# Performance work log

Measured on AMD Instinct MI355X. Metric: run time of the kernel, lower is better.

## Reference

```python
import jax, jax.numpy as jnp
import numpy as np

B, T, TRAIN = 4, 2048, 1536
D, H, L, FF, V = 512, 8, 12, 2048, 100
DH = D // H
ROPE_BASE = 100000.0


def layer_norm(x, g, b, eps=1e-5):
    mu = jnp.mean(x, axis=-1, keepdims=True)
    var = jnp.mean(jnp.square(x - mu), axis=-1, keepdims=True)
    return (x - mu) * jax.lax.rsqrt(var + eps) * g + b


def rope_cos_sin(t, dh):
    inv_freq = 1.0 / (ROPE_BASE ** (jnp.arange(0, dh, 2, dtype=jnp.float32) / dh))  # (dh/2,)
    ang = jnp.arange(t, dtype=jnp.float32)[:, None] * inv_freq[None, :]  # (T, dh/2)
    return jnp.cos(ang), jnp.sin(ang)


def apply_rope_interleaved(x, cos, sin):
    # x: (B, T, H, DH); interleaved pairs (x0,x1),(x2,x3),...
    x1, x2 = x[..., 0::2], x[..., 1::2]
    c, s = cos[None, :, None, :], sin[None, :, None, :]
    r1 = x1 * c - x2 * s
    r2 = x1 * s + x2 * c
    return jnp.stack([r1, r2], axis=-1).reshape(x.shape)


def setup_inputs() -> dict:
    key = jax.random.key(0)
    ks = jax.random.split(key, 20)
    sc = 0.02
    inp = {
        'R': jax.random.normal(ks[0], (B, T, D), jnp.float32),
        'y_train': jax.random.randint(ks[1], (B, TRAIN), 0, V),
        'emb': jax.random.normal(ks[2], (V, D), jnp.float32) * sc,
        'Wqkv': jax.random.normal(ks[3], (L, D, 3 * D), jnp.float32) * sc,
        'bqkv': jnp.zeros((L, 3 * D), jnp.float32),
        'Wo': jax.random.normal(ks[4], (L, D, D), jnp.float32) * sc,
        'bo': jnp.zeros((L, D), jnp.float32),
        'ln1_g': jnp.ones((L, D), jnp.float32),
        'ln1_b': jnp.zeros((L, D), jnp.float32),
        'ln2_g': jnp.ones((L, D), jnp.float32),
        'ln2_b': jnp.zeros((L, D), jnp.float32),
        'W1': jax.random.normal(ks[5], (L, D, FF), jnp.float32) * sc,
        'b1': jnp.zeros((L, FF), jnp.float32),
        'W2': jax.random.normal(ks[6], (L, FF, D), jnp.float32) * sc,
        'b2': jnp.zeros((L, D), jnp.float32),
        'pW1': jax.random.normal(ks[7], (D, 2 * D), jnp.float32) * sc,
        'pb1': jnp.zeros((2 * D,), jnp.float32),
        'pW2': jax.random.normal(ks[8], (2 * D, V), jnp.float32) * sc,
        'pb2': jnp.zeros((V,), jnp.float32),
    }
    return inp


def icl_forward(R, y_train, emb, Wqkv, bqkv, Wo, bo, ln1_g, ln1_b, ln2_g, ln2_b, W1, b1, W2, b2, pW1, pb1, pW2, pb2):
    b, t, d = R.shape
    train = y_train.shape[1]
    # label embedding: train rows get emb[y], test rows get zeros
    y_emb = jnp.concatenate([emb[y_train], jnp.zeros((b, t - train, d), R.dtype)], axis=1)
    rep = R + y_emb
    # ICL mask: column j visible iff j < train or j == i
    idx = jnp.arange(t)
    allowed = (idx[None, :] < train) | (idx[:, None] == idx[None, :])
    mask = jnp.where(allowed, 0.0, -jnp.inf).astype(R.dtype)  # (T, T)
    cos, sin = rope_cos_sin(t, DH)
    scale = 1.0 / jnp.sqrt(jnp.asarray(DH, R.dtype))

    def block(x, p):
        wqkv, bq, wo, bob, g1, be1, g2, be2, w1, bb1, w2, bb2 = p
        h = layer_norm(x, g1, be1)
        qkv = h @ wqkv + bq  # (B,T,3D)
        q, k, v = jnp.split(qkv, 3, axis=-1)
        q = q.reshape(b, t, H, DH)
        k = k.reshape(b, t, H, DH)
        v = v.reshape(b, t, H, DH)
        q = apply_rope_interleaved(q, cos, sin)
        k = apply_rope_interleaved(k, cos, sin)
        scores = jnp.einsum('bthd,bshd->bhts', q, k) * scale + mask
        attn = jax.nn.softmax(scores, axis=-1)
        o = jnp.einsum('bhts,bshd->bthd', attn, v).reshape(b, t, d)
        x = x + o @ wo + bob
        h2 = layer_norm(x, g2, be2)
        x = x + jax.nn.gelu(h2 @ w1 + bb1) @ w2 + bb2
        return x, None

    rep, _ = jax.lax.scan(block, rep, (Wqkv, bqkv, Wo, bo, ln1_g, ln1_b, ln2_g, ln2_b, W1, b1, W2, b2))
    test = rep[:, train:, :]
    logits = jax.nn.gelu(test @ pW1 + pb1) @ pW2 + pb2  # (B, test, V)
    return logits


def reference(R, y_train, emb, Wqkv, bqkv, Wo, bo, ln1_g, ln1_b, ln2_g, ln2_b, W1, b1, W2, b2, pW1, pb1, pW2, pb2):
    return icl_forward(R, y_train, emb, Wqkv, bqkv, Wo, bo, ln1_g, ln1_b, ln2_g, ln2_b, W1, b1, W2, b2, pW1, pb1, pW2, pb2)
```

## Files before the change

### kernel.cpp

```cpp
#include <hip/hip_runtime.h>
#include <hip/hip_bf16.h>

#define BB 4
#define TT 2048
#define TRAIN 1536
#define DD 512
#define HH 8
#define LL 12
#define FFD 2048
#define VV 100
#define DH 64
#define NT (BB*TT)
#define NTEST (BB*(TT-TRAIN))

typedef __bf16 bf16x8 __attribute__((ext_vector_type(8)));
typedef float  f32x4  __attribute__((ext_vector_type(4)));

#define GLDS16(g, l) __builtin_amdgcn_global_load_lds( \
    (const __attribute__((address_space(1))) void*)(g), \
    (__attribute__((address_space(3))) void*)(l), 16, 0, 0)

__global__ __launch_bounds__(256) void emb_add(const float* __restrict__ R,
                                               const int* __restrict__ y,
                                               const float* __restrict__ emb,
                                               float* __restrict__ rep) {
    int idx = blockIdx.x * 256 + threadIdx.x;
    int d = idx & 511;
    int n = idx >> 9;
    int t = n & (TT - 1);
    int b = n >> 11;
    float val = R[idx];
    if (t < TRAIN) {
        int tok = y[b * TRAIN + t];
        val += emb[(size_t)tok * DD + d];
    }
    rep[idx] = val;
}

__global__ __launch_bounds__(256) void ln_wave(const float* __restrict__ x,
                                               const float* __restrict__ g,
                                               const float* __restrict__ bta,
                                               __bf16* __restrict__ out) {
    int row = blockIdx.x * 4 + (threadIdx.x >> 6);
    int lane = threadIdx.x & 63;
    const float* xr = x + (size_t)row * DD + lane * 8;
    float4 a = *(const float4*)xr;
    float4 c = *(const float4*)(xr + 4);
    float s  = a.x + a.y + a.z + a.w + c.x + c.y + c.z + c.w;
    float sq = a.x*a.x + a.y*a.y + a.z*a.z + a.w*a.w + c.x*c.x + c.y*c.y + c.z*c.z + c.w*c.w;
#pragma unroll
    for (int off = 1; off < 64; off <<= 1) {
        s  += __shfl_xor(s, off);
        sq += __shfl_xor(sq, off);
    }
    float mu  = s * (1.0f / DD);
    float var = sq * (1.0f / DD) - mu * mu;
    float inv = rsqrtf(var + 1e-5f);
    const float* gp = g + lane * 8;
    const float* bp = bta + lane * 8;
    float4 g0 = *(const float4*)gp, g1 = *(const float4*)(gp + 4);
    float4 b0 = *(const float4*)bp, b1 = *(const float4*)(bp + 4);
    __bf16 o8[8];
    o8[0] = (__bf16)((a.x - mu) * inv * g0.x + b0.x);
    o8[1] = (__bf16)((a.y - mu) * inv * g0.y + b0.y);
    o8[2] = (__bf16)((a.z - mu) * inv * g0.z + b0.z);
    o8[3] = (__bf16)((a.w - mu) * inv * g0.w + b0.w);
    o8[4] = (__bf16)((c.x - mu) * inv * g1.x + b1.x);
    o8[5] = (__bf16)((c.y - mu) * inv * g1.y + b1.y);
    o8[6] = (__bf16)((c.z - mu) * inv * g1.z + b1.z);
    o8[7] = (__bf16)((c.w - mu) * inv * g1.w + b1.w);
    *(uint4*)(out + (size_t)row * DD + lane * 8) = *(uint4*)o8;
}

__global__ __launch_bounds__(256) void rope_tab(float* __restrict__ ctab, float* __restrict__ stab) {
    int idx = blockIdx.x * 256 + threadIdx.x;
    int p = idx & 31, t = idx >> 5;
    double freq = exp(-((double)(2 * p) / 64.0) * log(100000.0));
    double ang = (double)t * freq;
    ctab[idx] = (float)cos(ang);
    stab[idx] = (float)sin(ang);
}

__global__ __launch_bounds__(256) void rope_vt(const __bf16* __restrict__ qkv,
                                               const float* __restrict__ ctab,
                                               const float* __restrict__ stab,
                                               __bf16* __restrict__ qo,
                                               __bf16* __restrict__ ko,
                                               __bf16* __restrict__ vt) {
    int bh = blockIdx.y; int b = bh >> 3, h = bh & 7;
    int t0 = blockIdx.x * 64;
    __shared__ __bf16 tile[64][72];
    int tid = threadIdx.x;
    {
        int r = tid >> 2, cg = (tid & 3) * 16;
        const __bf16* src = qkv + (size_t)(b * TT + t0 + r) * (3 * DD) + 2 * DD + h * DH + cg;
        *(uint4*)&tile[r][cg]     = *(const uint4*)&src[0];
        *(uint4*)&tile[r][cg + 8] = *(const uint4*)&src[8];
    }
#pragma unroll
    for (int c = 0; c < 8; ++c) {
        int pidx = c * 256 + tid;
        int tl = pidx >> 5, p = pidx & 31;
        int t = t0 + tl;
        const __bf16* base = qkv + (size_t)(b * TT + t) * (3 * DD) + h * DH;
        float co = ctab[t * 32 + p], si = stab[t * 32 + p];
        float x1 = (float)base[2 * p],       x2 = (float)base[2 * p + 1];
        float k1 = (float)base[DD + 2 * p], k2 = (float)base[DD + 2 * p + 1];
        size_t ob = ((size_t)bh * TT + t) * DH;
        qo[ob + 2 * p]     = (__bf16)(x1 * co - x2 * si);
        qo[ob + 2 * p + 1] = (__bf16)(x1 * si + x2 * co);
        ko[ob + 2 * p]     = (__bf16)(k1 * co - k2 * si);
        ko[ob + 2 * p + 1] = (__bf16)(k1 * si + k2 * co);
    }
    __syncthreads();
    {
        int dh = tid >> 2, tg = (tid & 3) * 16;
        __bf16 outv[16];
#pragma unroll
        for (int j = 0; j < 16; ++j) outv[j] = tile[tg + j][dh];
        __bf16* dst = vt + ((size_t)bh * DH + dh) * TT + t0 + tg;
        *(uint4*)&dst[0] = *(uint4*)&outv[0];
        *(uint4*)&dst[8] = *(uint4*)&outv[8];
    }
}

#define KS_STRIDE 72
#define PS_STRIDE 136
#define VT_STRIDE 136

__global__ __launch_bounds__(512, 4) void attn_mfma(const __bf16* __restrict__ q,
                                                    const __bf16* __restrict__ k,
                                                    const __bf16* __restrict__ vt,
                                                    __bf16* __restrict__ obuf) {
    __shared__ __align__(16) __bf16 KPs[128 * PS_STRIDE];
    __shared__ __align__(16) __bf16 Vt[64 * VT_STRIDE];
    __shared__ float sself[128];

    const int tid = threadIdx.x;
    const int bh = blockIdx.y;
    const int b = bh >> 3, hh = bh & 7;
    const size_t kbase = (size_t)bh * TT * DH;
    const int t0q = blockIdx.x * 128;
    const int w = tid >> 6;
    const int lane = tid & 63;
    const int l16 = lane & 15;
    const int quad = lane >> 4;

    bf16x8 qa[2];
    {
        const __bf16* qg = q + kbase + (size_t)(t0q + w * 16 + l16) * DH + quad * 8;
#pragma unroll
        for (int ks = 0; ks < 2; ++ks) {
            uint4 u = *(const uint4*)&qg[ks * 32];
            const __bf16* pb = (const __bf16*)&u;
            bf16x8 vq;
#pragma unroll
            for (int j = 0; j < 8; ++j) vq[j] = (__bf16)((float)pb[j] * 0.125f);
            qa[ks] = vq;
        }
    }

    f32x4 oa[4] = {};
    float lst[4] = {};

    const int krow = tid >> 2, kc = (tid & 3) * 16;
    const int vdh = tid >> 3, vc = (tid & 7) * 16;

    for (int ci = 0; ci < TRAIN / 128; ++ci) {
        __syncthreads();
        {
            const __bf16* kg = k + kbase + (size_t)(ci * 128 + krow) * DH + kc;
            *(uint4*)&KPs[krow * KS_STRIDE + kc]     = *(const uint4*)&kg[0];
            *(uint4*)&KPs[krow * KS_STRIDE + kc + 8] = *(const uint4*)&kg[8];
            const __bf16* vg = vt + kbase + (size_t)vdh * TT + ci * 128 + vc;
            *(uint4*)&Vt[vdh * VT_STRIDE + vc]     = *(const uint4*)&vg[0];
            *(uint4*)&Vt[vdh * VT_STRIDE + vc + 8] = *(const uint4*)&vg[8];
        }
        __syncthreads();

        f32x4 acc[8] = {};
#pragma unroll
        for (int ks = 0; ks < 2; ++ks) {
            bf16x8 kb[8];
#pragma unroll
            for (int ni = 0; ni < 8; ++ni)
                kb[ni] = *(const bf16x8*)&KPs[(ni * 16 + l16) * KS_STRIDE + quad * 8 + ks * 32];
#pragma unroll
            for (int ni = 0; ni < 8; ++ni)
                acc[ni] = __builtin_amdgcn_mfma_f32_16x16x32_bf16(qa[ks], kb[ni], acc[ni], 0, 0, 0);
        }

#pragma unroll
        for (int r = 0; r < 4; ++r) {
            float rs = 0.f;
#pragma unroll
            for (int ni = 0; ni < 8; ++ni) {
                float pv = __expf(acc[ni][r]);
                acc[ni][r] = pv;
                rs += pv;
            }
            rs += __shfl_xor(rs, 1);
            rs += __shfl_xor(rs, 2);
            rs += __shfl_xor(rs, 4);
            rs += __shfl_xor(rs, 8);
            lst[r] += rs;
        }

        __syncthreads();
#pragma unroll
        for (int ni = 0; ni < 8; ++ni)
#pragma unroll
            for (int r = 0; r < 4; ++r)
                KPs[(w * 16 + quad * 4 + r) * PS_STRIDE + ((ni * 16 + l16) ^ (quad << 4))] = (__bf16)acc[ni][r];
        __syncthreads();

        const int psw = ((l16 >> 2) & 3) << 4;
#pragma unroll
        for (int ks = 0; ks < 4; ++ks) {
            bf16x8 pa = *(const bf16x8*)&KPs[(w * 16 + l16) * PS_STRIDE + ((ks * 32 + quad * 8) ^ psw)];
            bf16x8 vb[4];
#pragma unroll
            for (int ni = 0; ni < 4; ++ni)
                vb[ni] = *(const bf16x8*)&Vt[(ni * 16 + l16) * VT_STRIDE + quad * 8 + ks * 32];
#pragma unroll
            for (int ni = 0; ni < 4; ++ni)
                oa[ni] = __builtin_amdgcn_mfma_f32_16x16x32_bf16(pa, vb[ni], oa[ni], 0, 0, 0);
        }
    }

    if (t0q >= TRAIN) {
        __syncthreads();
        {
            const __bf16* vg = vt + kbase + (size_t)vdh * TT + t0q + vc;
            *(uint4*)&Vt[vdh * VT_STRIDE + vc]     = *(const uint4*)&vg[0];
            *(uint4*)&Vt[vdh * VT_STRIDE + vc + 8] = *(const uint4*)&vg[8];
            int row = tid >> 2, d0 = (tid & 3) * 16;
            const __bf16* qp = q + kbase + (size_t)(t0q + row) * DH + d0;
            const __bf16* kp = k + kbase + (size_t)(t0q + row) * DH + d0;
            float dacc = 0.f;
#pragma unroll
            for (int c = 0; c < 2; ++c) {
                uint4 uq = *(const uint4*)&qp[c * 8];
                uint4 uk = *(const uint4*)&kp[c * 8];
                const __bf16* pq = (const __bf16*)&uq;
                const __bf16* pk = (const __bf16*)&uk;
#pragma unroll
                for (int j = 0; j < 8; ++j) dacc += (float)pq[j] * (float)pk[j];
            }
            dacc += __shfl_xor(dacc, 1);
            dacc += __shfl_xor(dacc, 2);
            sself[row] = dacc * 0.125f;
        }
        __syncthreads();
#pragma unroll
        for (int r = 0; r < 4; ++r) {
            int row = w * 16 + quad * 4 + r;
            float pp = __expf(sself[row]);
            lst[r] += pp;
#pragma unroll
            for (int ni = 0; ni < 4; ++ni)
                oa[ni][r] += pp * (float)Vt[(ni * 16 + l16) * VT_STRIDE + row];
        }
    }

#pragma unroll
    for (int r = 0; r < 4; ++r) {
        float inv = 1.f / lst[r];
        int trow = t0q + w * 16 + quad * 4 + r;
        __bf16* op = obuf + ((size_t)(b * TT) + trow) * DD + hh * 64;
#pragma unroll
        for (int ni = 0; ni < 4; ++ni)
            op[ni * 16 + l16] = (__bf16)(oa[ni][r] * inv);
    }
}

__global__ __launch_bounds__(256) void transpose_pad(const float* __restrict__ src,
                                                     __bf16* __restrict__ dst,
                                                     int K, int N) {
    __shared__ __bf16 t[32][33];
    int n0 = blockIdx.x * 32, k0 = blockIdx.y * 32;
    int tx = threadIdx.x & 31, ty = threadIdx.x >> 5;
#pragma unroll
    for (int i = 0; i < 4; ++i) {
        int nn = n0 + tx;
        t[ty + i * 8][tx] = (nn < N) ? (__bf16)src[(size_t)(k0 + ty + i * 8) * N + nn] : (__bf16)0.f;
    }
    __syncthreads();
#pragma unroll
    for (int i = 0; i < 4; ++i) {
        dst[(size_t)(n0 + ty + i * 8) * K + k0 + tx] = t[tx][ty + i * 8];
    }
}

__global__ __launch_bounds__(256) void transpose_all(const float* __restrict__ s0,
                                                     const float* __restrict__ s1,
                                                     const float* __restrict__ s2,
                                                     const float* __restrict__ s3,
                                                     __bf16* __restrict__ d0, __bf16* __restrict__ d1,
                                                     __bf16* __restrict__ d2, __bf16* __restrict__ d3) {
    int i = blockIdx.x;
    const float* src; __bf16* dst; int K, N, tx, ty;
    if (i < 768)       { src = s0; dst = d0; K = 512;  N = 1536; int j = i;        tx = j % 48; ty = j / 48; }
    else if (i < 1024) { src = s1; dst = d1; K = 512;  N = 512;  int j = i - 768;  tx = j % 16; ty = j / 16; }
    else if (i < 2048) { src = s2; dst = d2; K = 512;  N = 2048; int j = i - 1024; tx = j % 64; ty = j / 64; }
    else               { src = s3; dst = d3; K = 2048; N = 512;  int j = i - 2048; tx = j % 16; ty = j / 16; }
    __shared__ __bf16 t[32][33];
    int n0 = tx * 32, k0 = ty * 32;
    int lx = threadIdx.x & 31, ly = threadIdx.x >> 5;
#pragma unroll
    for (int c = 0; c < 4; ++c)
        t[ly + c * 8][lx] = (__bf16)src[(size_t)(k0 + ly + c * 8) * N + n0 + lx];
    __syncthreads();
#pragma unroll
    for (int c = 0; c < 4; ++c)
        dst[(size_t)(n0 + ly + c * 8) * K + k0 + lx] = t[lx][ly + c * 8];
}

template <int EP, int TN>
__global__ __launch_bounds__(256) void gemm_bt(const __bf16* __restrict__ A,
                                               const __bf16* __restrict__ Bt,
                                               const float* __restrict__ bias,
                                               float* __restrict__ resid,
                                               __bf16* __restrict__ Cout,
                                               int M, int N, int K) {
    constexpr int NI = TN / 32;
    __shared__ __align__(16) __bf16 As[2][128 * 32];
    __shared__ __align__(16) __bf16 Bs[2][TN * 32];
    const int tid = threadIdx.x;
    const int m0 = blockIdx.x * 128;
    const int n0 = blockIdx.y * TN;
    const int lane = tid & 63;
    const int w = tid >> 6;
    const int wm = (w >> 1) * 64, wn = (w & 1) * (TN / 2);
    const int lrow = lane & 15;
    const int kq = (lane >> 4) * 8;

    f32x4 acc[4][NI] = {};

    const int srA = w * 32 + (lane >> 2);
    const int srB = w * (TN / 4) + (lane >> 2);
    const int scol = (lane & 3) * 8;
    const __bf16* gA = A  + (size_t)(m0 + srA) * K + scol;
    const __bf16* gB = Bt + (size_t)(n0 + srB) * K + scol;
    __bf16* lA0 = &As[0][(w * 32) * 32];
    __bf16* lA0b = lA0 + 16 * 32;
    __bf16* lA1 = &As[1][(w * 32) * 32];
    __bf16* lA1b = lA1 + 16 * 32;
    __bf16* lB0 = &Bs[0][(w * (TN / 4)) * 32];
    __bf16* lB1 = &Bs[1][(w * (TN / 4)) * 32];

    const int nk = K >> 6;
    for (int kt = 0; kt < nk; ++kt) {
        const int k0 = kt << 6;
        GLDS16(gA + k0,            lA0);
        GLDS16(gA + 16 * K + k0,   lA0b);
        GLDS16(gA + k0 + 32,       lA1);
        GLDS16(gA + 16 * K + k0 + 32, lA1b);
        GLDS16(gB + k0,            lB0);
        GLDS16(gB + k0 + 32,       lB1);
        if constexpr (TN == 128) {
            GLDS16(gB + 16 * K + k0,      lB0 + 16 * 32);
            GLDS16(gB + 16 * K + k0 + 32, lB1 + 16 * 32);
        }
        __syncthreads();
#pragma unroll
        for (int ps = 0; ps < 2; ++ps) {
            bf16x8 afr[4], bfr[NI];
#pragma unroll
            for (int i = 0; i < 4; ++i)
                afr[i] = *(const bf16x8*)&As[ps][(wm + i * 16 + lrow) * 32 + kq];
#pragma unroll
            for (int i = 0; i < NI; ++i)
                bfr[i] = *(const bf16x8*)&Bs[ps][(wn + i * 16 + lrow) * 32 + kq];
#pragma unroll
            for (int mi = 0; mi < 4; ++mi)
#pragma unroll
                for (int ni = 0; ni < NI; ++ni)
                    acc[mi][ni] = __builtin_amdgcn_mfma_f32_16x16x32_bf16(afr[mi], bfr[ni], acc[mi][ni], 0, 0, 0);
        }
        __syncthreads();
    }

    const int crow = (lane >> 4) * 4;
    const int ccol = lane & 15;
#pragma unroll
    for (int mi = 0; mi < 4; ++mi) {
#pragma unroll
        for (int ni = 0; ni < NI; ++ni) {
            int gn = n0 + wn + ni * 16 + ccol;
            float bv = bias[gn];
#pragma unroll
            for (int r = 0; r < 4; ++r) {
                int gm = m0 + wm + mi * 16 + crow + r;
                float vvv = acc[mi][ni][r] + bv;
                if constexpr (EP == 1) {
                    float x = vvv;
                    vvv = x / (1.f + __expf(-1.5957691216f * (x + 0.044715f * x * x * x)));
                }
                if constexpr (EP == 2) {
                    resid[(size_t)gm * N + gn] += vvv;
                } else if constexpr (EP == 4) {
                    if (gn < VV) resid[(size_t)gm * VV + gn] = vvv;
                } else {
                    Cout[(size_t)gm * N + gn] = (__bf16)vvv;
                }
            }
        }
    }
}

__global__ __launch_bounds__(256) void cast_test(const float* __restrict__ rep, __bf16* __restrict__ testb) {
    int idx = blockIdx.x * 256 + threadIdx.x;
    int d = idx & 511;
    int i = idx >> 9;
    int ttk = i & 511;
    int b = i >> 9;
    testb[idx] = (__bf16)rep[(size_t)(b * TT + TRAIN + ttk) * DD + d];
}

__global__ void pad_bias(const float* __restrict__ pb2, float* __restrict__ pb2p) {
    int t = threadIdx.x;
    if (t < 128) pb2p[t] = (t < VV) ? pb2[t] : 0.f;
}

extern "C" void kernel_launch(void* const* d_in, const int* in_sizes, int n_in,
                              void* d_out, int out_size, void* d_ws, size_t ws_size,
                              hipStream_t stream) {
    const float* R    = (const float*)d_in[0];
    const int*   y    = (const int*)d_in[1];
    const float* emb  = (const float*)d_in[2];
    const float* Wqkv = (const float*)d_in[3];
    const float* bqkv = (const float*)d_in[4];
    const float* Wo   = (const float*)d_in[5];
    const float* bo   = (const float*)d_in[6];
    const float* ln1g = (const float*)d_in[7];
    const float* ln1b = (const float*)d_in[8];
    const float* ln2g = (const float*)d_in[9];
    const float* ln2b = (const float*)d_in[10];
    const float* W1   = (const float*)d_in[11];
    const float* b1   = (const float*)d_in[12];
    const float* W2   = (const float*)d_in[13];
    const float* b2   = (const float*)d_in[14];
    const float* pW1  = (const float*)d_in[15];
    const float* pb1  = (const float*)d_in[16];
    const float* pW2  = (const float*)d_in[17];
    const float* pb2  = (const float*)d_in[18];

    char* p = (char*)d_ws;
    float* rep    = (float*)p;  p += (size_t)NT * DD * 4;
    __bf16* hbuf  = (__bf16*)p; p += (size_t)NT * DD * 2;
    __bf16* qkv   = (__bf16*)p;
    __bf16* ffb   = qkv;        p += (size_t)NT * FFD * 2;
    __bf16* qb    = (__bf16*)p; p += (size_t)NT * DD * 2;
    __bf16* kb    = (__bf16*)p; p += (size_t)NT * DD * 2;
    __bf16* vtb   = (__bf16*)p; p += (size_t)NT * DD * 2;
    __bf16* obuf  = (__bf16*)p; p += (size_t)NT * DD * 2;
    __bf16* wqkvT = (__bf16*)p; p += (size_t)1536 * 512 * 2;
    __bf16* woT   = (__bf16*)p; p += (size_t)512 * 512 * 2;
    __bf16* w1T   = (__bf16*)p; p += (size_t)2048 * 512 * 2;
    __bf16* w2T   = (__bf16*)p; p += (size_t)512 * 2048 * 2;
    float* ctab   = (float*)p;  p += (size_t)TT * 32 * 4;
    float* stab   = (float*)p;  p += (size_t)TT * 32 * 4;
    float* pb2p   = (float*)p;  p += 512;
    __bf16* testb = hbuf;
    __bf16* hb    = obuf;

    emb_add<<<NT * DD / 256, 256, 0, stream>>>(R, y, emb, rep);
    rope_tab<<<TT * 32 / 256, 256, 0, stream>>>(ctab, stab);

    for (int l = 0; l < LL; ++l) {
        ln_wave<<<NT / 4, 256, 0, stream>>>(rep, ln1g + l * DD, ln1b + l * DD, hbuf);
        transpose_all<<<3072, 256, 0, stream>>>(Wqkv + (size_t)l * DD * 3 * DD, Wo + (size_t)l * DD * DD,
                                                W1 + (size_t)l * DD * FFD, W2 + (size_t)l * FFD * DD,
                                                wqkvT, woT, w1T, w2T);
        gemm_bt<0, 128><<<dim3(NT / 128, 1536 / 128), 256, 0, stream>>>(hbuf, wqkvT, bqkv + l * 3 * DD, nullptr, qkv, NT, 3 * DD, DD);
        rope_vt<<<dim3(TT / 64, BB * HH), 256, 0, stream>>>(qkv, ctab, stab, qb, kb, vtb);
        attn_mfma<<<dim3(TT / 128, BB * HH), 512, 0, stream>>>(qb, kb, vtb, obuf);
        gemm_bt<2, 64><<<dim3(NT / 128, 512 / 64), 256, 0, stream>>>(obuf, woT, bo + l * DD, rep, nullptr, NT, DD, DD);
        ln_wave<<<NT / 4, 256, 0, stream>>>(rep, ln2g + l * DD, ln2b + l * DD, hbuf);
        gemm_bt<1, 128><<<dim3(NT / 128, FFD / 128), 256, 0, stream>>>(hbuf, w1T, b1 + l * FFD, nullptr, ffb, NT, FFD, DD);
        gemm_bt<2, 64><<<dim3(NT / 128, 512 / 64), 256, 0, stream>>>(ffb, w2T, b2 + l * DD, rep, nullptr, NT, DD, FFD);
    }

    cast_test<<<NTEST * DD / 256, 256, 0, stream>>>(rep, testb);
    transpose_pad<<<dim3(1024 / 32, 512 / 32), 256, 0, stream>>>(pW1, w1T, DD, 2 * DD);
    gemm_bt<1, 64><<<dim3(NTEST / 128, 1024 / 64), 256, 0, stream>>>(testb, w1T, pb1, nullptr, hb, NTEST, 2 * DD, DD);
    pad_bias<<<1, 128, 0, stream>>>(pb2, pb2p);
    transpose_pad<<<dim3(128 / 32, 1024 / 32), 256, 0, stream>>>(pW2, w2T, 2 * DD, VV);
    gemm_bt<4, 128><<<dim3(NTEST / 128, 1), 256, 0, stream>>>(hb, w2T, pb2p, (float*)d_out, nullptr, NTEST, 128, 2 * DD);
}
```

Measured before the change: 2.522 ms.

## Restructure attention kernel: 256-query tiles, async double-buffered K loads, swizzled LDS

The attention kernel now gives each block 256 query rows, two 16-row sub-tiles per wave, so every K/V chunk in LDS is reused across twice as many queries. K chunks are double-buffered and loaded with global_load_lds direct-to-LDS copies using XOR swizzles. The S matrix is computed transposed (K as the A operand), so P can be written to LDS as packed 4-element stores, and s_setprio is raised around the MFMA sections. The aim is to cut global-load and LDS traffic and to hide load latency. In exchange the grid has half as many blocks (256 total), and the larger LDS and register footprint lowers occupancy.

```diff
diff --git a/kernel.cpp b/kernel.cpp
--- a/kernel.cpp
+++ b/kernel.cpp
@@ -124,154 +124,190 @@
     }
 }
 
-#define KS_STRIDE 72
-#define PS_STRIDE 136
-#define VT_STRIDE 136
-
-__global__ __launch_bounds__(512, 4) void attn_mfma(const __bf16* __restrict__ q,
+#define NCH (TRAIN/128)
+#define PSE 136
+
+__global__ __launch_bounds__(512, 2) void attn_mfma(const __bf16* __restrict__ q,
                                                     const __bf16* __restrict__ k,
                                                     const __bf16* __restrict__ vt,
                                                     __bf16* __restrict__ obuf) {
-    __shared__ __align__(16) __bf16 KPs[128 * PS_STRIDE];
-    __shared__ __align__(16) __bf16 Vt[64 * VT_STRIDE];
-    __shared__ float sself[128];
+    __shared__ __align__(16) __bf16 Kb[2][128 * 64];
+    __shared__ __align__(16) __bf16 Vb[64 * 128];
+    __shared__ __align__(16) __bf16 Pb[256 * PSE];
+    __shared__ float sself[256];
 
     const int tid = threadIdx.x;
     const int bh = blockIdx.y;
     const int b = bh >> 3, hh = bh & 7;
     const size_t kbase = (size_t)bh * TT * DH;
-    const int t0q = blockIdx.x * 128;
+    const int t0q = blockIdx.x * 256;
     const int w = tid >> 6;
     const int lane = tid & 63;
     const int l16 = lane & 15;
     const int quad = lane >> 4;
-
-    bf16x8 qa[2];
-    {
-        const __bf16* qg = q + kbase + (size_t)(t0q + w * 16 + l16) * DH + quad * 8;
+    const int x7 = l16 & 7;
+
+    bf16x8 qa[2][2];
+#pragma unroll
+    for (int mi = 0; mi < 2; ++mi)
 #pragma unroll
         for (int ks = 0; ks < 2; ++ks) {
-            uint4 u = *(const uint4*)&qg[ks * 32];
+            const __bf16* qg = q + kbase + (size_t)(t0q + w * 32 + mi * 16 + l16) * DH + ks * 32 + quad * 8;
+            uint4 u = *(const uint4*)qg;
             const __bf16* pb = (const __bf16*)&u;
             bf16x8 vq;
 #pragma unroll
             for (int j = 0; j < 8; ++j) vq[j] = (__bf16)((float)pb[j] * 0.125f);
-            qa[ks] = vq;
-        }
-    }
-
-    f32x4 oa[4] = {};
-    float lst[4] = {};
-
-    const int krow = tid >> 2, kc = (tid & 3) * 16;
-    const int vdh = tid >> 3, vc = (tid & 7) * 16;
-
-    for (int ci = 0; ci < TRAIN / 128; ++ci) {
+            qa[mi][ks] = vq;
+        }
+
+    const int krl = lane >> 3, ksl = lane & 7;
+    const int vrl = lane >> 4, vsl = lane & 15;
+
+    f32x4 oa[2][4] = {};
+    float lsum[2] = {0.f, 0.f};
+
+    {
+        const __bf16* g = k + kbase;
+#pragma unroll
+        for (int c = 0; c < 2; ++c) {
+            int rb = w * 2 + c;
+            GLDS16(g + (size_t)(rb * 8 + krl) * DH + ((ksl ^ krl) * 8), &Kb[0][rb * 512]);
+        }
+    }
+
+    for (int ci = 0; ci < NCH; ++ci) {
         __syncthreads();
         {
-            const __bf16* kg = k + kbase + (size_t)(ci * 128 + krow) * DH + kc;
-            *(uint4*)&KPs[krow * KS_STRIDE + kc]     = *(const uint4*)&kg[0];
-            *(uint4*)&KPs[krow * KS_STRIDE + kc + 8] = *(const uint4*)&kg[8];
-            const __bf16* vg = vt + kbase + (size_t)vdh * TT + ci * 128 + vc;
-            *(uint4*)&Vt[vdh * VT_STRIDE + vc]     = *(const uint4*)&vg[0];
-            *(uint4*)&Vt[vdh * VT_STRIDE + vc + 8] = *(const uint4*)&vg[8];
-        }
+#pragma unroll
+            for (int c = 0; c < 2; ++c) {
+                int rb = w * 2 + c;
+                int dh = rb * 4 + vrl;
+                GLDS16(vt + kbase + (size_t)dh * TT + ci * 128 + ((vsl ^ (dh & 7)) * 8), &Vb[rb * 512]);
+            }
+        }
+
+        const __bf16* kc = Kb[ci & 1];
+        f32x4 acc[2][8] = {};
+        __builtin_amdgcn_s_setprio(1);
+#pragma unroll
+        for (int ks = 0; ks < 2; ++ks) {
+            bf16x8 kf[8];
+#pragma unroll
+            for (int ni = 0; ni < 8; ++ni)
+                kf[ni] = *(const bf16x8*)&kc[(ni * 16 + l16) * 64 + (((ks * 4 + quad) ^ x7) * 8)];
+#pragma unroll
+            for (int ni = 0; ni < 8; ++ni) {
+                acc[0][ni] = __builtin_amdgcn_mfma_f32_16x16x32_bf16(kf[ni], qa[0][ks], acc[0][ni], 0, 0, 0);
+                acc[1][ni] = __builtin_amdgcn_mfma_f32_16x16x32_bf16(kf[ni], qa[1][ks], acc[1][ni], 0, 0, 0);
+            }
+        }
+        __builtin_amdgcn_s_setprio(0);
+
+#pragma unroll
+        for (int mi = 0; mi < 2; ++mi) {
+            float rs = 0.f;
+#pragma unroll
+            for (int ni = 0; ni < 8; ++ni) {
+                float p0 = __expf(acc[mi][ni][0]);
+                float p1 = __expf(acc[mi][ni][1]);
+                float p2 = __expf(acc[mi][ni][2]);
+                float p3 = __expf(acc[mi][ni][3]);
+                rs += (p0 + p1) + (p2 + p3);
+                __bf16 p4[4] = {(__bf16)p0, (__bf16)p1, (__bf16)p2, (__bf16)p3};
+                *(uint2*)&Pb[(w * 32 + mi * 16 + l16) * PSE + ni * 16 + quad * 4] = *(const uint2*)p4;
+            }
+            rs += __shfl_xor(rs, 16);
+            rs += __shfl_xor(rs, 32);
+            lsum[mi] += rs;
+        }
+
         __syncthreads();
-
-        f32x4 acc[8] = {};
-#pragma unroll
-        for (int ks = 0; ks < 2; ++ks) {
-            bf16x8 kb[8];
-#pragma unroll
-            for (int ni = 0; ni < 8; ++ni)
-                kb[ni] = *(const bf16x8*)&KPs[(ni * 16 + l16) * KS_STRIDE + quad * 8 + ks * 32];
-#pragma unroll
-            for (int ni = 0; ni < 8; ++ni)
-                acc[ni] = __builtin_amdgcn_mfma_f32_16x16x32_bf16(qa[ks], kb[ni], acc[ni], 0, 0, 0);
-        }
-
-#pragma unroll
-        for (int r = 0; r < 4; ++r) {
-            float rs = 0.f;
-#pragma unroll
-            for (int ni = 0; ni < 8; ++ni) {
-                float pv = __expf(acc[ni][r]);
-                acc[ni][r] = pv;
-                rs += pv;
-            }
-            rs += __shfl_xor(rs, 1);
-            rs += __shfl_xor(rs, 2);
-            rs += __shfl_xor(rs, 4);
-            rs += __shfl_xor(rs, 8);
-            lst[r] += rs;
-        }
-
-        __syncthreads();
-#pragma unroll
-        for (int ni = 0; ni < 8; ++ni)
-#pragma unroll
-            for (int r = 0; r < 4; ++r)
-                KPs[(w * 16 + quad * 4 + r) * PS_STRIDE + ((ni * 16 + l16) ^ (quad << 4))] = (__bf16)acc[ni][r];
-        __syncthreads();
-
-        const int psw = ((l16 >> 2) & 3) << 4;
+        if (ci + 1 < NCH) {
+            const __bf16* g = k + kbase + (size_t)((ci + 1) * 128) * DH;
+            __bf16* dst = Kb[(ci + 1) & 1];
+#pragma unroll
+            for (int c = 0; c < 2; ++c) {
+                int rb = w * 2 + c;
+                GLDS16(g + (size_t)(rb * 8 + krl) * DH + ((ksl ^ krl) * 8), dst + rb * 512);
+            }
+        }
+
+        __builtin_amdgcn_s_setprio(1);
 #pragma unroll
         for (int ks = 0; ks < 4; ++ks) {
-            bf16x8 pa = *(const bf16x8*)&KPs[(w * 16 + l16) * PS_STRIDE + ((ks * 32 + quad * 8) ^ psw)];
-            bf16x8 vb[4];
+            bf16x8 vf[4];
 #pragma unroll
             for (int ni = 0; ni < 4; ++ni)
-                vb[ni] = *(const bf16x8*)&Vt[(ni * 16 + l16) * VT_STRIDE + quad * 8 + ks * 32];
-#pragma unroll
-            for (int ni = 0; ni < 4; ++ni)
-                oa[ni] = __builtin_amdgcn_mfma_f32_16x16x32_bf16(pa, vb[ni], oa[ni], 0, 0, 0);
-        }
-    }
+                vf[ni] = *(const bf16x8*)&Vb[(ni * 16 + l16) * 128 + (((ks * 4 + quad) ^ x7) * 8)];
+            bf16x8 pa0 = *(const bf16x8*)&Pb[(w * 32 + l16) * PSE + ks * 32 + quad * 8];
+            bf16x8 pa1 = *(const bf16x8*)&Pb[(w * 32 + 16 + l16) * PSE + ks * 32 + quad * 8];
+#pragma unroll
+            for (int ni = 0; ni < 4; ++ni) {
+                oa[0][ni] = __builtin_amdgcn_mfma_f32_16x16x32_bf16(pa0, vf[ni], oa[0][ni], 0, 0, 0);
+                oa[1][ni] = __builtin_amdgcn_mfma_f32_16x16x32_bf16(pa1, vf[ni], oa[1][ni], 0, 0, 0);
+            }
+        }
+        __builtin_amdgcn_s_setprio(0);
+    }
+
+    float lr[2][4];
+#pragma unroll
+    for (int mi = 0; mi < 2; ++mi)
+#pragma unroll
+        for (int r = 0; r < 4; ++r)
+            lr[mi][r] = __shfl(lsum[mi], quad * 4 + r);
 
     if (t0q >= TRAIN) {
+        __bf16* selfV = &Kb[0][0];
         __syncthreads();
         {
-            const __bf16* vg = vt + kbase + (size_t)vdh * TT + t0q + vc;
-            *(uint4*)&Vt[vdh * VT_STRIDE + vc]     = *(const uint4*)&vg[0];
-            *(uint4*)&Vt[vdh * VT_STRIDE + vc + 8] = *(const uint4*)&vg[8];
-            int row = tid >> 2, d0 = (tid & 3) * 16;
-            const __bf16* qp = q + kbase + (size_t)(t0q + row) * DH + d0;
-            const __bf16* kp = k + kbase + (size_t)(t0q + row) * DH + d0;
+            int dh = tid >> 3, c0 = (tid & 7) * 32;
+            const __bf16* vg = vt + kbase + (size_t)dh * TT + t0q + c0;
+#pragma unroll
+            for (int u = 0; u < 4; ++u)
+                *(uint4*)&selfV[dh * 256 + c0 + u * 8] = *(const uint4*)&vg[u * 8];
+            int row = tid >> 1, hf = tid & 1;
+            const __bf16* qp = q + kbase + (size_t)(t0q + row) * DH + hf * 32;
+            const __bf16* kp = k + kbase + (size_t)(t0q + row) * DH + hf * 32;
             float dacc = 0.f;
 #pragma unroll
-            for (int c = 0; c < 2; ++c) {
-                uint4 uq = *(const uint4*)&qp[c * 8];
-                uint4 uk = *(const uint4*)&kp[c * 8];
+            for (int u = 0; u < 4; ++u) {
+                uint4 uq = *(const uint4*)&qp[u * 8];
+                uint4 uk = *(const uint4*)&kp[u * 8];
                 const __bf16* pq = (const __bf16*)&uq;
                 const __bf16* pk = (const __bf16*)&uk;
 #pragma unroll
                 for (int j = 0; j < 8; ++j) dacc += (float)pq[j] * (float)pk[j];
             }
             dacc += __shfl_xor(dacc, 1);
-            dacc += __shfl_xor(dacc, 2);
             sself[row] = dacc * 0.125f;
         }
         __syncthreads();
 #pragma unroll
+        for (int mi = 0; mi < 2; ++mi)
+#pragma unroll
+            for (int r = 0; r < 4; ++r) {
+                int qr = w * 32 + mi * 16 + quad * 4 + r;
+                float pp = __expf(sself[qr]);
+                lr[mi][r] += pp;
+#pragma unroll
+                for (int ni = 0; ni < 4; ++ni)
+                    oa[mi][ni][r] += pp * (float)selfV[(ni * 16 + l16) * 256 + qr];
+            }
+    }
+
+#pragma unroll
+    for (int mi = 0; mi < 2; ++mi)
+#pragma unroll
         for (int r = 0; r < 4; ++r) {
-            int row = w * 16 + quad * 4 + r;
-            float pp = __expf(sself[row]);
-            lst[r] += pp;
+            float inv = 1.f / lr[mi][r];
+            int trow = t0q + w * 32 + mi * 16 + quad * 4 + r;
+            __bf16* op = obuf + ((size_t)(b * TT) + trow) * DD + hh * 64;
 #pragma unroll
             for (int ni = 0; ni < 4; ++ni)
-                oa[ni][r] += pp * (float)Vt[(ni * 16 + l16) * VT_STRIDE + row];
-        }
-    }
-
-#pragma unroll
-    for (int r = 0; r < 4; ++r) {
-        float inv = 1.f / lst[r];
-        int trow = t0q + w * 16 + quad * 4 + r;
-        __bf16* op = obuf + ((size_t)(b * TT) + trow) * DD + hh * 64;
-#pragma unroll
-        for (int ni = 0; ni < 4; ++ni)
-            op[ni * 16 + l16] = (__bf16)(oa[ni][r] * inv);
-    }
+                op[ni * 16 + l16] = (__bf16)(oa[mi][ni][r] * inv);
+        }
 }
 
 __global__ __launch_bounds__(256) void transpose_pad(const float* __restrict__ src,
@@ -475,7 +511,7 @@
                                                 wqkvT, woT, w1T, w2T);
         gemm_bt<0, 128><<<dim3(NT / 128, 1536 / 128), 256, 0, stream>>>(hbuf, wqkvT, bqkv + l * 3 * DD, nullptr, qkv, NT, 3 * DD, DD);
         rope_vt<<<dim3(TT / 64, BB * HH), 256, 0, stream>>>(qkv, ctab, stab, qb, kb, vtb);
-        attn_mfma<<<dim3(TT / 128, BB * HH), 512, 0, stream>>>(qb, kb, vtb, obuf);
+        attn_mfma<<<dim3(TT / 256, BB * HH), 512, 0, stream>>>(qb, kb, vtb, obuf);
         gemm_bt<2, 64><<<dim3(NT / 128, 512 / 64), 256, 0, stream>>>(obuf, woT, bo + l * DD, rep, nullptr, NT, DD, DD);
         ln_wave<<<NT / 4, 256, 0, stream>>>(rep, ln2g + l * DD, ln2b + l * DD, hbuf);
         gemm_bt<1, 128><<<dim3(NT / 128, FFD / 128), 256, 0, stream>>>(hbuf, w1T, b1 + l * FFD, nullptr, ffb, NT, FFD, DD);
```

Result: faster. 2.337 ms (-7.3%).
